# Kernel tuning notes

Measured on AMD Instinct MI355X. Metric: run time of the kernel, lower is better.

The kernel has to match this reference:

```python
import jax, jax.numpy as jnp
import numpy as np

KEY_DIM = 1024
SCALE = KEY_DIM ** -0.5


def setup_inputs() -> dict:
    key = jax.random.key(0)
    k1, k2, k3, k4 = jax.random.split(key, 4)
    B, S, E = 4, 2048, 1024
    x = jax.random.normal(k1, (B, S, E), dtype=jnp.float32)
    WQ = jax.random.normal(k2, (KEY_DIM, E), dtype=jnp.float32) * (E ** -0.5)
    WK = jax.random.normal(k3, (KEY_DIM, E), dtype=jnp.float32) * (E ** -0.5)
    WV = jax.random.normal(k4, (KEY_DIM, E), dtype=jnp.float32) * (E ** -0.5)
    return {"x": x, "WQ": WQ, "WK": WK, "WV": WV}


def reference(x, WQ, WK, WV):
    # x: [B, S, E]; Linear(bias=False) weights are [out, in] as in torch.
    q = jnp.einsum('bse,ke->bsk', x, WQ)   # [B, S, K]
    k = jnp.einsum('bse,ke->bsk', x, WK)   # [B, S, K]
    v = jnp.einsum('bse,ve->bsv', x, WV)   # [B, S, V]
    scores = jnp.einsum('bsk,btk->bst', q, k) * SCALE  # [B, S, S]
    # Faithful to torch: mask where tril(scores) == 0 (upper triangle).
    masked = jnp.where(jnp.tril(scores) == 0, -jnp.inf, scores)
    attn = jax.nn.softmax(masked, axis=-1)
    return jnp.einsum('bst,btv->bsv', attn, v)  # dropout=0.0 -> identity
```

## Files before the change

kernel.cpp:

```cpp
#include <hip/hip_runtime.h>

typedef _Float16 f16x8 __attribute__((ext_vector_type(8)));
typedef unsigned short u16x8v __attribute__((ext_vector_type(8)));
typedef unsigned short u16x4v __attribute__((ext_vector_type(4)));
typedef float f32x4 __attribute__((ext_vector_type(4)));

constexpr int SEQ = 2048;
constexpr int DIM = 1024;
constexpr int BATCH = 4;
constexpr size_t NBS = (size_t)BATCH * SEQ * DIM;

static __device__ __forceinline__ unsigned short f2h(float f) {
    return __builtin_bit_cast(unsigned short, (_Float16)f);
}
static __device__ __forceinline__ float h2f(unsigned short u) {
    return (float)__builtin_bit_cast(_Float16, u);
}
static __device__ __forceinline__ f16x8 ldsld(const unsigned short* p) {
    return __builtin_bit_cast(f16x8, *(const u16x8v*)p);
}
static __device__ __forceinline__ void gld_lds16(const unsigned short* g, unsigned short* l) {
    __builtin_amdgcn_global_load_lds(
        (const __attribute__((address_space(1))) void*)g,
        (__attribute__((address_space(3))) void*)l, 16, 0, 0);
}

__global__ __launch_bounds__(256) void cvt_f16(
    const float* __restrict__ in, unsigned short* __restrict__ out, int n4)
{
    int i = blockIdx.x * 256 + threadIdx.x;
    if (i >= n4) return;
    float4 f = ((const float4*)in)[i];
    u16x4v h;
    h.x = f2h(f.x); h.y = f2h(f.y); h.z = f2h(f.z); h.w = f2h(f.w);
    ((u16x4v*)out)[i] = h;
}

__global__ __launch_bounds__(256) void qkv_gemm(
    const unsigned short* __restrict__ Xf, const unsigned short* __restrict__ Wf,
    unsigned short* __restrict__ Qf, unsigned short* __restrict__ Kf,
    unsigned short* __restrict__ Vt)
{
    __shared__ __attribute__((aligned(16))) unsigned short Ah[128 * 32];
    __shared__ __attribute__((aligned(16))) unsigned short Bh[128 * 32];
    const int m0 = blockIdx.x * 128, n0 = blockIdx.y * 128, z = blockIdx.z;
    const unsigned short* Wz = Wf + (size_t)z * DIM * DIM;
    const int tid = threadIdx.x;
    const int w = tid >> 6, lane = tid & 63, q = lane >> 4, c = lane & 15;
    const int wrow = (w >> 1) * 64, wcol = (w & 1) * 64;
    const int grow = w * 32 + (lane >> 2);
    const int gcol = (lane & 3) * 8;
    unsigned short* lA = Ah + w * 1024;
    unsigned short* lB = Bh + w * 1024;

    f32x4 acc[4][4];
#pragma unroll
    for (int a = 0; a < 4; ++a)
#pragma unroll
        for (int b = 0; b < 4; ++b) acc[a][b] = (f32x4){0.f, 0.f, 0.f, 0.f};

    for (int k0 = 0; k0 < DIM; k0 += 32) {
        __syncthreads();
        {
            const size_t ga = (size_t)(m0 + grow) * DIM + k0 + gcol;
            const size_t gb = (size_t)(n0 + grow) * DIM + k0 + gcol;
            gld_lds16(Xf + ga, lA);
            gld_lds16(Xf + ga + (size_t)16 * DIM, lA + 512);
            gld_lds16(Wz + gb, lB);
            gld_lds16(Wz + gb + (size_t)16 * DIM, lB + 512);
        }
        __syncthreads();
        f16x8 ah[4], bh[4];
#pragma unroll
        for (int mi = 0; mi < 4; ++mi)
            ah[mi] = ldsld(Ah + (wrow + mi * 16 + c) * 32 + q * 8);
#pragma unroll
        for (int ni = 0; ni < 4; ++ni)
            bh[ni] = ldsld(Bh + (wcol + ni * 16 + c) * 32 + q * 8);
#pragma unroll
        for (int mi = 0; mi < 4; ++mi)
#pragma unroll
            for (int ni = 0; ni < 4; ++ni)
                acc[mi][ni] = __builtin_amdgcn_mfma_f32_16x16x32_f16(ah[mi], bh[ni], acc[mi][ni], 0, 0, 0);
    }

    if (z == 2) {
#pragma unroll
        for (int mi = 0; mi < 4; ++mi) {
            const int mg = m0 + wrow + mi * 16 + q * 4;
            const int bb = mg >> 11, ss = mg & (SEQ - 1);
#pragma unroll
            for (int ni = 0; ni < 4; ++ni) {
                const int col = n0 + wcol + ni * 16 + c;
                u16x4v v;
                v.x = f2h(acc[mi][ni][0]);
                v.y = f2h(acc[mi][ni][1]);
                v.z = f2h(acc[mi][ni][2]);
                v.w = f2h(acc[mi][ni][3]);
                *(u16x4v*)(Vt + ((size_t)bb * DIM + col) * SEQ + ss) = v;
            }
        }
    } else {
        unsigned short* OH = z ? Kf : Qf;
#pragma unroll
        for (int mi = 0; mi < 4; ++mi)
#pragma unroll
            for (int ni = 0; ni < 4; ++ni) {
                const int col = n0 + wcol + ni * 16 + c;
#pragma unroll
                for (int r = 0; r < 4; ++r) {
                    const int row = m0 + wrow + mi * 16 + q * 4 + r;
                    OH[(size_t)row * DIM + col] = f2h(acc[mi][ni][r]);
                }
            }
    }
}

__global__ __launch_bounds__(256) void scores_gemm1b(
    const unsigned short* __restrict__ Q, const unsigned short* __restrict__ K,
    unsigned short* __restrict__ S)
{
    if (blockIdx.y > blockIdx.x) return;
    __shared__ __attribute__((aligned(16))) unsigned short Ah[128 * 32];
    __shared__ __attribute__((aligned(16))) unsigned short Bh[128 * 32];
    const int i0 = blockIdx.x * 128, j0 = blockIdx.y * 128, b = blockIdx.z;
    const unsigned short* Qb = Q + (size_t)b * SEQ * DIM;
    const unsigned short* Kb = K + (size_t)b * SEQ * DIM;
    unsigned short* Sb = S + (size_t)b * SEQ * SEQ;
    const int tid = threadIdx.x;
    const int w = tid >> 6, lane = tid & 63, q = lane >> 4, c = lane & 15;
    const int wrow = (w >> 1) * 64, wcol = (w & 1) * 64;
    const int grow = w * 32 + (lane >> 2);
    const int gcol = (lane & 3) * 8;
    unsigned short* lA = Ah + w * 1024;
    unsigned short* lB = Bh + w * 1024;

    f32x4 acc[4][4];
#pragma unroll
    for (int a = 0; a < 4; ++a)
#pragma unroll
        for (int bq = 0; bq < 4; ++bq) acc[a][bq] = (f32x4){0.f, 0.f, 0.f, 0.f};

    for (int k0 = 0; k0 < DIM; k0 += 32) {
        __syncthreads();
        {
            const size_t ga = (size_t)(i0 + grow) * DIM + k0 + gcol;
            const size_t gb = (size_t)(j0 + grow) * DIM + k0 + gcol;
            gld_lds16(Qb + ga, lA);
            gld_lds16(Qb + ga + (size_t)16 * DIM, lA + 512);
            gld_lds16(Kb + gb, lB);
            gld_lds16(Kb + gb + (size_t)16 * DIM, lB + 512);
        }
        __syncthreads();
        f16x8 ah[4], bh[4];
#pragma unroll
        for (int mi = 0; mi < 4; ++mi)
            ah[mi] = ldsld(Ah + (wrow + mi * 16 + c) * 32 + q * 8);
#pragma unroll
        for (int ni = 0; ni < 4; ++ni)
            bh[ni] = ldsld(Bh + (wcol + ni * 16 + c) * 32 + q * 8);
#pragma unroll
        for (int mi = 0; mi < 4; ++mi)
#pragma unroll
            for (int ni = 0; ni < 4; ++ni)
                acc[mi][ni] = __builtin_amdgcn_mfma_f32_16x16x32_f16(ah[mi], bh[ni], acc[mi][ni], 0, 0, 0);
    }
#pragma unroll
    for (int mi = 0; mi < 4; ++mi)
#pragma unroll
        for (int ni = 0; ni < 4; ++ni) {
            const int col = j0 + wcol + ni * 16 + c;
#pragma unroll
            for (int r = 0; r < 4; ++r) {
                const int row = i0 + wrow + mi * 16 + q * 4 + r;
                const float sc = acc[mi][ni][r] * 0.03125f;
                Sb[(size_t)row * SEQ + col] =
                    (sc == 0.f) ? (unsigned short)0xFC00u : f2h(sc);
            }
        }
}

__global__ __launch_bounds__(256) void softmax_row_b(
    const unsigned short* __restrict__ S, unsigned short* __restrict__ P)
{
    const int i = blockIdx.x, t = threadIdx.x;
    const size_t ro = ((size_t)blockIdx.y * SEQ + i) * SEQ;
    const int wid = t >> 6, lane = t & 63;
    __shared__ float redm[4], reds[4];
    const int j0 = t * 8;
    u16x8v raw = *(const u16x8v*)(S + ro + j0);
    float sv[8];
    float mx = -__builtin_inff();
#pragma unroll
    for (int u = 0; u < 8; ++u) {
        float s = (j0 + u <= i) ? h2f(raw[u]) : -__builtin_inff();
        sv[u] = s;
        mx = fmaxf(mx, s);
    }
#pragma unroll
    for (int off = 1; off < 64; off <<= 1) mx = fmaxf(mx, __shfl_xor(mx, off));
    if (lane == 0) redm[wid] = mx;
    __syncthreads();
    const float M = fmaxf(fmaxf(redm[0], redm[1]), fmaxf(redm[2], redm[3]));
    float sum = 0.f;
#pragma unroll
    for (int u = 0; u < 8; ++u) {
        float e = __expf(sv[u] - M);
        sv[u] = e;
        sum += e;
    }
#pragma unroll
    for (int off = 1; off < 64; off <<= 1) sum += __shfl_xor(sum, off);
    if (lane == 0) reds[wid] = sum;
    __syncthreads();
    const float rinv = 1.f / (reds[0] + reds[1] + reds[2] + reds[3]);
    u16x8v o;
#pragma unroll
    for (int u = 0; u < 8; ++u) o[u] = f2h(sv[u] * rinv);
    *(u16x8v*)(P + ro + j0) = o;
}

__global__ __launch_bounds__(256) void pv_gemm(
    const unsigned short* __restrict__ Pm, const unsigned short* __restrict__ Vt,
    float* __restrict__ Out)
{
    __shared__ __attribute__((aligned(16))) unsigned short Ps[128 * 32];
    __shared__ __attribute__((aligned(16))) unsigned short Vs[128 * 32];
    const int i0 = blockIdx.x * 128, d0 = blockIdx.y * 128, b = blockIdx.z;
    const int tid = threadIdx.x;
    const int w = tid >> 6, lane = tid & 63, q = lane >> 4, c = lane & 15;
    const int wrow = (w >> 1) * 64, wcol = (w & 1) * 64;
    const int grow = w * 32 + (lane >> 2);
    const int gcol = (lane & 3) * 8;
    unsigned short* lA = Ps + w * 1024;
    unsigned short* lB = Vs + w * 1024;

    f32x4 acc[4][4];
#pragma unroll
    for (int a = 0; a < 4; ++a)
#pragma unroll
        for (int bq = 0; bq < 4; ++bq) acc[a][bq] = (f32x4){0.f, 0.f, 0.f, 0.f};

    const int njs = i0 / 32 + 4;

    for (int ks = 0; ks < njs; ++ks) {
        const int j0 = ks * 32;
        __syncthreads();
        {
            const unsigned short* gp = Pm + ((size_t)b * SEQ + i0 + grow) * SEQ + j0 + gcol;
            const unsigned short* gv = Vt + ((size_t)b * DIM + d0 + grow) * SEQ + j0 + gcol;
            gld_lds16(gp, lA);
            gld_lds16(gp + (size_t)16 * SEQ, lA + 512);
            gld_lds16(gv, lB);
            gld_lds16(gv + (size_t)16 * SEQ, lB + 512);
        }
        __syncthreads();
        f16x8 ah[4], bh[4];
#pragma unroll
        for (int mi = 0; mi < 4; ++mi)
            ah[mi] = ldsld(Ps + (wrow + mi * 16 + c) * 32 + q * 8);
#pragma unroll
        for (int ni = 0; ni < 4; ++ni)
            bh[ni] = ldsld(Vs + (wcol + ni * 16 + c) * 32 + q * 8);
#pragma unroll
        for (int mi = 0; mi < 4; ++mi)
#pragma unroll
            for (int ni = 0; ni < 4; ++ni)
                acc[mi][ni] = __builtin_amdgcn_mfma_f32_16x16x32_f16(ah[mi], bh[ni], acc[mi][ni], 0, 0, 0);
    }
#pragma unroll
    for (int mi = 0; mi < 4; ++mi)
#pragma unroll
        for (int ni = 0; ni < 4; ++ni) {
            const int dcol = d0 + wcol + ni * 16 + c;
#pragma unroll
            for (int r = 0; r < 4; ++r) {
                const int i = i0 + wrow + mi * 16 + q * 4 + r;
                Out[((size_t)b * SEQ + i) * DIM + dcol] = acc[mi][ni][r];
            }
        }
}

extern "C" void kernel_launch(void* const* d_in, const int* in_sizes, int n_in,
                              void* d_out, int out_size, void* d_ws, size_t ws_size,
                              hipStream_t stream)
{
    (void)out_size; (void)ws_size;
    const float* X = nullptr;
    const float* Wv[3] = {nullptr, nullptr, nullptr};
    int nw = 0;
    for (int i = 0; i < n_in; ++i) {
        if (in_sizes[i] == (int)NBS)
            X = (const float*)d_in[i];
        else if (nw < 3)
            Wv[nw++] = (const float*)d_in[i];
    }

    unsigned short* ws = (unsigned short*)d_ws;
    unsigned short* Qf = ws;
    unsigned short* Kf = ws + NBS;
    unsigned short* Vt = ws + 2 * NBS;
    unsigned short* Xf = ws + 3 * NBS;
    unsigned short* Pp = ws + 3 * NBS;
    unsigned short* Sb = ws + 5 * NBS;
    unsigned short* Wf = ws + 7 * NBS;
    float* Out = (float*)d_out;

    cvt_f16<<<dim3((int)(NBS / 4 / 256)), 256, 0, stream>>>(X, Xf, (int)(NBS / 4));
    const int wn4 = DIM * DIM / 4;
    for (int z = 0; z < 3; ++z)
        cvt_f16<<<dim3(wn4 / 256), 256, 0, stream>>>(
            Wv[z], Wf + (size_t)z * DIM * DIM, wn4);

    qkv_gemm<<<dim3(64, 8, 3), 256, 0, stream>>>(Xf, Wf, Qf, Kf, Vt);

    scores_gemm1b<<<dim3(16, 16, BATCH), 256, 0, stream>>>(Qf, Kf, Sb);
    softmax_row_b<<<dim3(SEQ, BATCH), 256, 0, stream>>>(Sb, Pp);

    pv_gemm<<<dim3(16, 8, BATCH), 256, 0, stream>>>(Pp, Vt, Out);
}
```

Measured before the change: 277.9 us.

## Double K-tile depth with XOR-swizzled LDS, merge conversions, skip masked softmax work

```diff
diff --git a/kernel.cpp b/kernel.cpp
--- a/kernel.cpp
+++ b/kernel.cpp
@@ -25,33 +25,52 @@
         (__attribute__((address_space(3))) void*)l, 16, 0, 0);
 }
 
-__global__ __launch_bounds__(256) void cvt_f16(
-    const float* __restrict__ in, unsigned short* __restrict__ out, int n4)
-{
-    int i = blockIdx.x * 256 + threadIdx.x;
-    if (i >= n4) return;
-    float4 f = ((const float4*)in)[i];
+__global__ __launch_bounds__(256) void cvt_all(
+    const float* __restrict__ X,
+    const float* __restrict__ W0, const float* __restrict__ W1,
+    const float* __restrict__ W2,
+    unsigned short* __restrict__ Xf, unsigned short* __restrict__ Wf)
+{
+    const int b = blockIdx.x;
+    const float* src;
+    unsigned short* dst;
+    int i;
+    if (b < 8192) {
+        src = X; dst = Xf;
+        i = b * 256 + threadIdx.x;
+    } else {
+        const int wb = b - 8192;
+        const int z = wb >> 10;
+        src = (z == 0) ? W0 : (z == 1) ? W1 : W2;
+        dst = Wf + (size_t)z * DIM * DIM;
+        i = (wb & 1023) * 256 + threadIdx.x;
+    }
+    float4 f = ((const float4*)src)[i];
     u16x4v h;
     h.x = f2h(f.x); h.y = f2h(f.y); h.z = f2h(f.z); h.w = f2h(f.w);
-    ((u16x4v*)out)[i] = h;
-}
+    ((u16x4v*)dst)[i] = h;
+}
+
 
 __global__ __launch_bounds__(256) void qkv_gemm(
     const unsigned short* __restrict__ Xf, const unsigned short* __restrict__ Wf,
     unsigned short* __restrict__ Qf, unsigned short* __restrict__ Kf,
     unsigned short* __restrict__ Vt)
 {
-    __shared__ __attribute__((aligned(16))) unsigned short Ah[128 * 32];
-    __shared__ __attribute__((aligned(16))) unsigned short Bh[128 * 32];
+    __shared__ __attribute__((aligned(16))) unsigned short Ah[128 * 64];
+    __shared__ __attribute__((aligned(16))) unsigned short Bh[128 * 64];
     const int m0 = blockIdx.x * 128, n0 = blockIdx.y * 128, z = blockIdx.z;
     const unsigned short* Wz = Wf + (size_t)z * DIM * DIM;
     const int tid = threadIdx.x;
     const int w = tid >> 6, lane = tid & 63, q = lane >> 4, c = lane & 15;
     const int wrow = (w >> 1) * 64, wcol = (w & 1) * 64;
-    const int grow = w * 32 + (lane >> 2);
-    const int gcol = (lane & 3) * 8;
-    unsigned short* lA = Ah + w * 1024;
-    unsigned short* lB = Bh + w * 1024;
+    const int g8 = lane >> 3;
+    const int cu = (lane & 7) ^ g8;
+    const int srow = w * 8 + g8;
+    const int scol = cu * 8;
+    unsigned short* lA = Ah + w * 512;
+    unsigned short* lB = Bh + w * 512;
+    const int c7 = c & 7;
 
     f32x4 acc[4][4];
 #pragma unroll
@@ -59,29 +78,33 @@
 #pragma unroll
         for (int b = 0; b < 4; ++b) acc[a][b] = (f32x4){0.f, 0.f, 0.f, 0.f};
 
-    for (int k0 = 0; k0 < DIM; k0 += 32) {
+    for (int k0 = 0; k0 < DIM; k0 += 64) {
         __syncthreads();
         {
-            const size_t ga = (size_t)(m0 + grow) * DIM + k0 + gcol;
-            const size_t gb = (size_t)(n0 + grow) * DIM + k0 + gcol;
-            gld_lds16(Xf + ga, lA);
-            gld_lds16(Xf + ga + (size_t)16 * DIM, lA + 512);
-            gld_lds16(Wz + gb, lB);
-            gld_lds16(Wz + gb + (size_t)16 * DIM, lB + 512);
-        }
-        __syncthreads();
-        f16x8 ah[4], bh[4];
-#pragma unroll
-        for (int mi = 0; mi < 4; ++mi)
-            ah[mi] = ldsld(Ah + (wrow + mi * 16 + c) * 32 + q * 8);
-#pragma unroll
-        for (int ni = 0; ni < 4; ++ni)
-            bh[ni] = ldsld(Bh + (wcol + ni * 16 + c) * 32 + q * 8);
-#pragma unroll
-        for (int mi = 0; mi < 4; ++mi)
+            const size_t ga = (size_t)(m0 + srow) * DIM + k0 + scol;
+            const size_t gb = (size_t)(n0 + srow) * DIM + k0 + scol;
+#pragma unroll
+            for (int j = 0; j < 4; ++j) {
+                gld_lds16(Xf + ga + (size_t)(j * 32) * DIM, lA + j * 2048);
+                gld_lds16(Wz + gb + (size_t)(j * 32) * DIM, lB + j * 2048);
+            }
+        }
+        __syncthreads();
+#pragma unroll
+        for (int kk = 0; kk < 2; ++kk) {
+            f16x8 ah[4], bh[4];
+#pragma unroll
+            for (int mi = 0; mi < 4; ++mi)
+                ah[mi] = ldsld(Ah + (wrow + mi * 16 + c) * 64 + (((kk << 2) + q) ^ c7) * 8);
 #pragma unroll
             for (int ni = 0; ni < 4; ++ni)
-                acc[mi][ni] = __builtin_amdgcn_mfma_f32_16x16x32_f16(ah[mi], bh[ni], acc[mi][ni], 0, 0, 0);
+                bh[ni] = ldsld(Bh + (wcol + ni * 16 + c) * 64 + (((kk << 2) + q) ^ c7) * 8);
+#pragma unroll
+            for (int mi = 0; mi < 4; ++mi)
+#pragma unroll
+                for (int ni = 0; ni < 4; ++ni)
+                    acc[mi][ni] = __builtin_amdgcn_mfma_f32_16x16x32_f16(ah[mi], bh[ni], acc[mi][ni], 0, 0, 0);
+        }
     }
 
     if (z == 2) {
@@ -121,8 +144,8 @@
     unsigned short* __restrict__ S)
 {
     if (blockIdx.y > blockIdx.x) return;
-    __shared__ __attribute__((aligned(16))) unsigned short Ah[128 * 32];
-    __shared__ __attribute__((aligned(16))) unsigned short Bh[128 * 32];
+    __shared__ __attribute__((aligned(16))) unsigned short Ah[128 * 64];
+    __shared__ __attribute__((aligned(16))) unsigned short Bh[128 * 64];
     const int i0 = blockIdx.x * 128, j0 = blockIdx.y * 128, b = blockIdx.z;
     const unsigned short* Qb = Q + (size_t)b * SEQ * DIM;
     const unsigned short* Kb = K + (size_t)b * SEQ * DIM;
@@ -130,10 +153,13 @@
     const int tid = threadIdx.x;
     const int w = tid >> 6, lane = tid & 63, q = lane >> 4, c = lane & 15;
     const int wrow = (w >> 1) * 64, wcol = (w & 1) * 64;
-    const int grow = w * 32 + (lane >> 2);
-    const int gcol = (lane & 3) * 8;
-    unsigned short* lA = Ah + w * 1024;
-    unsigned short* lB = Bh + w * 1024;
+    const int g8 = lane >> 3;
+    const int cu = (lane & 7) ^ g8;
+    const int srow = w * 8 + g8;
+    const int scol = cu * 8;
+    unsigned short* lA = Ah + w * 512;
+    unsigned short* lB = Bh + w * 512;
+    const int c7 = c & 7;
 
     f32x4 acc[4][4];
 #pragma unroll
@@ -141,29 +167,33 @@
 #pragma unroll
         for (int bq = 0; bq < 4; ++bq) acc[a][bq] = (f32x4){0.f, 0.f, 0.f, 0.f};
 
-    for (int k0 = 0; k0 < DIM; k0 += 32) {
+    for (int k0 = 0; k0 < DIM; k0 += 64) {
         __syncthreads();
         {
-            const size_t ga = (size_t)(i0 + grow) * DIM + k0 + gcol;
-            const size_t gb = (size_t)(j0 + grow) * DIM + k0 + gcol;
-            gld_lds16(Qb + ga, lA);
-            gld_lds16(Qb + ga + (size_t)16 * DIM, lA + 512);
-            gld_lds16(Kb + gb, lB);
-            gld_lds16(Kb + gb + (size_t)16 * DIM, lB + 512);
-        }
-        __syncthreads();
-        f16x8 ah[4], bh[4];
-#pragma unroll
-        for (int mi = 0; mi < 4; ++mi)
-            ah[mi] = ldsld(Ah + (wrow + mi * 16 + c) * 32 + q * 8);
-#pragma unroll
-        for (int ni = 0; ni < 4; ++ni)
-            bh[ni] = ldsld(Bh + (wcol + ni * 16 + c) * 32 + q * 8);
-#pragma unroll
-        for (int mi = 0; mi < 4; ++mi)
+            const size_t ga = (size_t)(i0 + srow) * DIM + k0 + scol;
+            const size_t gb = (size_t)(j0 + srow) * DIM + k0 + scol;
+#pragma unroll
+            for (int j = 0; j < 4; ++j) {
+                gld_lds16(Qb + ga + (size_t)(j * 32) * DIM, lA + j * 2048);
+                gld_lds16(Kb + gb + (size_t)(j * 32) * DIM, lB + j * 2048);
+            }
+        }
+        __syncthreads();
+#pragma unroll
+        for (int kk = 0; kk < 2; ++kk) {
+            f16x8 ah[4], bh[4];
+#pragma unroll
+            for (int mi = 0; mi < 4; ++mi)
+                ah[mi] = ldsld(Ah + (wrow + mi * 16 + c) * 64 + (((kk << 2) + q) ^ c7) * 8);
 #pragma unroll
             for (int ni = 0; ni < 4; ++ni)
-                acc[mi][ni] = __builtin_amdgcn_mfma_f32_16x16x32_f16(ah[mi], bh[ni], acc[mi][ni], 0, 0, 0);
+                bh[ni] = ldsld(Bh + (wcol + ni * 16 + c) * 64 + (((kk << 2) + q) ^ c7) * 8);
+#pragma unroll
+            for (int mi = 0; mi < 4; ++mi)
+#pragma unroll
+                for (int ni = 0; ni < 4; ++ni)
+                    acc[mi][ni] = __builtin_amdgcn_mfma_f32_16x16x32_f16(ah[mi], bh[ni], acc[mi][ni], 0, 0, 0);
+        }
     }
 #pragma unroll
     for (int mi = 0; mi < 4; ++mi)
@@ -188,14 +218,20 @@
     const int wid = t >> 6, lane = t & 63;
     __shared__ float redm[4], reds[4];
     const int j0 = t * 8;
-    u16x8v raw = *(const u16x8v*)(S + ro + j0);
+    const int rti = (i & ~127) + 128;
     float sv[8];
     float mx = -__builtin_inff();
-#pragma unroll
-    for (int u = 0; u < 8; ++u) {
-        float s = (j0 + u <= i) ? h2f(raw[u]) : -__builtin_inff();
-        sv[u] = s;
-        mx = fmaxf(mx, s);
+    if (j0 <= i) {
+        u16x8v raw = *(const u16x8v*)(S + ro + j0);
+#pragma unroll
+        for (int u = 0; u < 8; ++u) {
+            float s = (j0 + u <= i) ? h2f(raw[u]) : -__builtin_inff();
+            sv[u] = s;
+            mx = fmaxf(mx, s);
+        }
+    } else {
+#pragma unroll
+        for (int u = 0; u < 8; ++u) sv[u] = -__builtin_inff();
     }
 #pragma unroll
     for (int off = 1; off < 64; off <<= 1) mx = fmaxf(mx, __shfl_xor(mx, off));
@@ -214,26 +250,31 @@
     if (lane == 0) reds[wid] = sum;
     __syncthreads();
     const float rinv = 1.f / (reds[0] + reds[1] + reds[2] + reds[3]);
-    u16x8v o;
-#pragma unroll
-    for (int u = 0; u < 8; ++u) o[u] = f2h(sv[u] * rinv);
-    *(u16x8v*)(P + ro + j0) = o;
+    if (j0 < rti) {
+        u16x8v o;
+#pragma unroll
+        for (int u = 0; u < 8; ++u) o[u] = f2h(sv[u] * rinv);
+        *(u16x8v*)(P + ro + j0) = o;
+    }
 }
 
 __global__ __launch_bounds__(256) void pv_gemm(
     const unsigned short* __restrict__ Pm, const unsigned short* __restrict__ Vt,
     float* __restrict__ Out)
 {
-    __shared__ __attribute__((aligned(16))) unsigned short Ps[128 * 32];
-    __shared__ __attribute__((aligned(16))) unsigned short Vs[128 * 32];
+    __shared__ __attribute__((aligned(16))) unsigned short Ps[128 * 64];
+    __shared__ __attribute__((aligned(16))) unsigned short Vs[128 * 64];
     const int i0 = blockIdx.x * 128, d0 = blockIdx.y * 128, b = blockIdx.z;
     const int tid = threadIdx.x;
     const int w = tid >> 6, lane = tid & 63, q = lane >> 4, c = lane & 15;
     const int wrow = (w >> 1) * 64, wcol = (w & 1) * 64;
-    const int grow = w * 32 + (lane >> 2);
-    const int gcol = (lane & 3) * 8;
-    unsigned short* lA = Ps + w * 1024;
-    unsigned short* lB = Vs + w * 1024;
+    const int g8 = lane >> 3;
+    const int cu = (lane & 7) ^ g8;
+    const int srow = w * 8 + g8;
+    const int scol = cu * 8;
+    unsigned short* lA = Ps + w * 512;
+    unsigned short* lB = Vs + w * 512;
+    const int c7 = c & 7;
 
     f32x4 acc[4][4];
 #pragma unroll
@@ -241,32 +282,36 @@
 #pragma unroll
         for (int bq = 0; bq < 4; ++bq) acc[a][bq] = (f32x4){0.f, 0.f, 0.f, 0.f};
 
-    const int njs = i0 / 32 + 4;
+    const int njs = i0 / 64 + 2;
 
     for (int ks = 0; ks < njs; ++ks) {
-        const int j0 = ks * 32;
+        const int j0 = ks * 64;
         __syncthreads();
         {
-            const unsigned short* gp = Pm + ((size_t)b * SEQ + i0 + grow) * SEQ + j0 + gcol;
-            const unsigned short* gv = Vt + ((size_t)b * DIM + d0 + grow) * SEQ + j0 + gcol;
-            gld_lds16(gp, lA);
-            gld_lds16(gp + (size_t)16 * SEQ, lA + 512);
-            gld_lds16(gv, lB);
-            gld_lds16(gv + (size_t)16 * SEQ, lB + 512);
-        }
-        __syncthreads();
-        f16x8 ah[4], bh[4];
-#pragma unroll
-        for (int mi = 0; mi < 4; ++mi)
-            ah[mi] = ldsld(Ps + (wrow + mi * 16 + c) * 32 + q * 8);
-#pragma unroll
-        for (int ni = 0; ni < 4; ++ni)
-            bh[ni] = ldsld(Vs + (wcol + ni * 16 + c) * 32 + q * 8);
-#pragma unroll
-        for (int mi = 0; mi < 4; ++mi)
+            const size_t gpa = ((size_t)b * SEQ + i0 + srow) * SEQ + j0 + scol;
+            const size_t gva = ((size_t)b * DIM + d0 + srow) * SEQ + j0 + scol;
+#pragma unroll
+            for (int j = 0; j < 4; ++j) {
+                gld_lds16(Pm + gpa + (size_t)(j * 32) * SEQ, lA + j * 2048);
+                gld_lds16(Vt + gva + (size_t)(j * 32) * SEQ, lB + j * 2048);
+            }
+        }
+        __syncthreads();
+#pragma unroll
+        for (int kk = 0; kk < 2; ++kk) {
+            f16x8 ah[4], bh[4];
+#pragma unroll
+            for (int mi = 0; mi < 4; ++mi)
+                ah[mi] = ldsld(Ps + (wrow + mi * 16 + c) * 64 + (((kk << 2) + q) ^ c7) * 8);
 #pragma unroll
             for (int ni = 0; ni < 4; ++ni)
-                acc[mi][ni] = __builtin_amdgcn_mfma_f32_16x16x32_f16(ah[mi], bh[ni], acc[mi][ni], 0, 0, 0);
+                bh[ni] = ldsld(Vs + (wcol + ni * 16 + c) * 64 + (((kk << 2) + q) ^ c7) * 8);
+#pragma unroll
+            for (int mi = 0; mi < 4; ++mi)
+#pragma unroll
+                for (int ni = 0; ni < 4; ++ni)
+                    acc[mi][ni] = __builtin_amdgcn_mfma_f32_16x16x32_f16(ah[mi], bh[ni], acc[mi][ni], 0, 0, 0);
+        }
     }
 #pragma unroll
     for (int mi = 0; mi < 4; ++mi)
@@ -306,11 +351,7 @@
     unsigned short* Wf = ws + 7 * NBS;
     float* Out = (float*)d_out;
 
-    cvt_f16<<<dim3((int)(NBS / 4 / 256)), 256, 0, stream>>>(X, Xf, (int)(NBS / 4));
-    const int wn4 = DIM * DIM / 4;
-    for (int z = 0; z < 3; ++z)
-        cvt_f16<<<dim3(wn4 / 256), 256, 0, stream>>>(
-            Wv[z], Wf + (size_t)z * DIM * DIM, wn4);
+    cvt_all<<<dim3(8192 + 3072), 256, 0, stream>>>(X, Wv[0], Wv[1], Wv[2], Xf, Wf);
 
     qkv_gemm<<<dim3(64, 8, 3), 256, 0, stream>>>(Xf, Wf, Qf, Kf, Vt);
 
```

Result: faster. 243.1 us (-12.5%).
